# Kernel optimization log

Measured on AMD Instinct MI355X. Metric: run time of the kernel, lower is better.

Reference implementation:

```python
import jax, jax.numpy as jnp
import numpy as np

N, E, D = 20000, 640000, 128  # nodes, edges, hidden_nf
ED = 3  # edge_feat_nf (1 input col + distance col + geodesic col)
NORM_FACTOR = 100.0
NORM_CONST = 1.0
LN_EPS = 1e-5


def setup_inputs() -> dict:
    key = jax.random.key(0)
    ks = jax.random.split(key, 24)
    w = lambda k, s: (jax.random.normal(k, s, dtype=jnp.float32) * 0.1)
    inp = {
        "h": jax.random.normal(ks[0], (N, D), dtype=jnp.float32),
        "x": jax.random.normal(ks[1], (N, 3), dtype=jnp.float32),
        "edge_index": jax.random.randint(ks[2], (2, E), 0, N),
        "node_mask": jnp.ones((N, 1), jnp.float32),
        "edge_mask": jnp.ones((E, 1), jnp.float32),
        "edge_attr": jax.random.uniform(ks[3], (E, 1), dtype=jnp.float32),
        # GCLayer params
        "W_lin": w(ks[4], (D, D)), "b_lin": jnp.zeros((D,), jnp.float32),
        "We1": w(ks[5], (D + ED, D)), "be1": jnp.zeros((D,), jnp.float32),
        "We2": w(ks[6], (D, D)), "be2": jnp.zeros((D,), jnp.float32),
        "Wn1": w(ks[7], (D, D)), "bn1": jnp.zeros((D,), jnp.float32),
        "Wn2": w(ks[8], (D, D)), "bn2": jnp.zeros((D,), jnp.float32),
        "Wa1": w(ks[9], (2 * D + ED, D)), "ba1": jnp.zeros((D,), jnp.float32),
        "Wa2": w(ks[10], (D, 1)), "ba2": jnp.zeros((1,), jnp.float32),
        "ln_g": jnp.ones((D,), jnp.float32), "ln_b": jnp.zeros((D,), jnp.float32),
        # EquivariantUpdate coord_mlp params (last layer bias-free, gain 0.001)
        "Wc1": w(ks[11], (2 * D + ED, D)), "bc1": jnp.zeros((D,), jnp.float32),
        "Wc2": w(ks[12], (D, D)), "bc2": jnp.zeros((D,), jnp.float32),
        "Wc3": w(ks[13], (D, 1)) * 0.01,
    }
    return inp


def _forward(h, x, edge_index, node_mask, edge_mask, edge_attr,
             W_lin, b_lin, We1, be1, We2, be2, Wn1, bn1, Wn2, bn2,
             Wa1, ba1, Wa2, ba2, ln_g, ln_b, Wc1, bc1, Wc2, bc2, Wc3):
    silu = jax.nn.silu
    row, col = edge_index[0], edge_index[1]
    # coord2diff
    diff = x[row] - x[col]                                     # [E,3]
    radial = jnp.sum(diff * diff, axis=1, keepdims=True)
    dist = jnp.sqrt(radial + 1e-8)                             # [E,1]
    coord_diff = diff / (dist + NORM_CONST)
    e = jnp.concatenate([dist, edge_attr], axis=1)             # [E,2]
    # ---- GCLayer (Euclidean reduction of HGCLayer) ----
    hh = h @ W_lin + b_lin                                     # [N,D]
    hr, hc = hh[row], hh[col]
    geo = jnp.sqrt(jnp.sum((hr - hc) ** 2, axis=1, keepdims=True) + 1e-8)
    e3 = jnp.concatenate([e, geo], axis=1)                     # [E,3]
    att_in = jnp.concatenate([hr, hc, e3], axis=1)             # [E,2D+3]
    att = jax.nn.sigmoid(silu(att_in @ Wa1 + ba1) @ Wa2 + ba2) * edge_mask
    msg_in = jnp.concatenate([hc - hr, e3], axis=1)            # [E,D+3]
    msg = (silu(msg_in @ We1 + be1) @ We2 + be2) * att
    agg = jax.ops.segment_sum(msg, row, num_segments=hh.shape[0])  # [N,D]
    out = silu(agg @ Wn1 + bn1) @ Wn2 + bn2
    hh = hh + out
    mu = jnp.mean(hh, axis=-1, keepdims=True)
    var = jnp.mean((hh - mu) ** 2, axis=-1, keepdims=True)
    hh = (hh - mu) * jax.lax.rsqrt(var + LN_EPS) * ln_g + ln_b
    hh = silu(hh)
    # ---- EquivariantUpdate (tanh=False) ----
    cin = jnp.concatenate([hh[row], hh[col], e3], axis=1)      # [E,2D+3]
    m = silu(cin @ Wc1 + bc1)
    m = silu(m @ Wc2 + bc2)
    m = m @ Wc3                                                # [E,1]
    trans = coord_diff * m * edge_mask
    aggx = jax.ops.segment_sum(trans, row, num_segments=x.shape[0]) / NORM_FACTOR
    x_out = (x + aggx) * node_mask
    return hh, x_out


def reference(h, x, edge_index, node_mask, edge_mask, edge_attr,
              W_lin, b_lin, We1, be1, We2, be2, Wn1, bn1, Wn2, bn2,
              Wa1, ba1, Wa2, ba2, ln_g, ln_b, Wc1, bc1, Wc2, bc2, Wc3):
    return _forward(h, x, edge_index, node_mask, edge_mask, edge_attr,
                    W_lin, b_lin, We1, be1, We2, be2, Wn1, bn1, Wn2, bn2,
                    Wa1, ba1, Wa2, ba2, ln_g, ln_b, Wc1, bc1, Wc2, bc2, Wc3)
```

## Files before the change

kernel.cpp:

```cpp
#include <hip/hip_runtime.h>
#include <hip/hip_bf16.h>


#define D 128
#define RS 136

typedef unsigned short ushort;
typedef __attribute__((ext_vector_type(8))) short short8;
typedef __attribute__((ext_vector_type(4))) float f32x4;

__device__ __forceinline__ float rcpf(float x) { return __builtin_amdgcn_rcpf(x); }
__device__ __forceinline__ float siluf(float x) { return x * rcpf(1.0f + __expf(-x)); }
__device__ __forceinline__ float sigmf(float x) { return rcpf(1.0f + __expf(-x)); }
__device__ __forceinline__ ushort f2bs(float f) {
    __hip_bfloat16 b = __float2bfloat16(f);
    ushort u; __builtin_memcpy(&u, &b, 2); return u;
}
__device__ __forceinline__ unsigned pkbf(float lo, float hi) {
    __hip_bfloat162 h2 = __float22bfloat162_rn(make_float2(lo, hi));
    unsigned u; __builtin_memcpy(&u, &h2, 4); return u;
}
#define MFMA16(a, b, c) __builtin_amdgcn_mfma_f32_16x16x32_bf16((a), (b), (c), 0, 0, 0)

#define PWLIN 0
#define PWA1  5
#define PWE1  14
#define PWE2  19
#define PWN1  23
#define PWN2  28
#define PWC1  32
#define PWC2  41
#define NPACK 45

__global__ void k_zero(float* __restrict__ p, long n) {
    long i = (long)blockIdx.x * blockDim.x + threadIdx.x;
    long stride = (long)gridDim.x * blockDim.x;
    for (; i < n; i += stride) p[i] = 0.0f;
}

__global__ void k_hist(const int* __restrict__ eidx, int* __restrict__ cnt, int E) {
    int i = blockIdx.x * blockDim.x + threadIdx.x;
    const int stride = gridDim.x * blockDim.x;
    for (; i < E; i += stride) atomicAdd(&cnt[eidx[i]], 1);
}

__global__ __launch_bounds__(1024) void k_scan(const int* __restrict__ cnt,
                                               int* __restrict__ cur, int N) {
    __shared__ int part[1024];
    const int t = threadIdx.x;
    const int chunk = (N + 1023) / 1024;
    int s = 0;
    for (int k = 0; k < chunk; ++k) {
        const int i = t * chunk + k;
        if (i < N) s += cnt[i];
    }
    part[t] = s;
    __syncthreads();
    for (int d = 1; d < 1024; d <<= 1) {
        const int v = (t >= d) ? part[t - d] : 0;
        __syncthreads();
        part[t] += v;
        __syncthreads();
    }
    int base = (t == 0) ? 0 : part[t - 1];
    for (int k = 0; k < chunk; ++k) {
        const int i = t * chunk + k;
        if (i < N) { cur[i] = base; base += cnt[i]; }
    }
}

__global__ void k_scatter_build(
    const int* __restrict__ eidx, const float* __restrict__ x,
    const float* __restrict__ eattr, const float* __restrict__ emask,
    int* __restrict__ cur, float4* __restrict__ rec, int E) {
    int i = blockIdx.x * blockDim.x + threadIdx.x;
    const int stride = gridDim.x * blockDim.x;
    for (; i < E; i += stride) {
        const int r = eidx[i], c = eidx[E + i];
        const int p = atomicAdd(&cur[r], 1);
        const float dx = x[r * 3 + 0] - x[c * 3 + 0];
        const float dy = x[r * 3 + 1] - x[c * 3 + 1];
        const float dz = x[r * 3 + 2] - x[c * 3 + 2];
        const float dist = sqrtf(dx * dx + dy * dy + dz * dz + 1e-8f);
        const float inv = rcpf(dist + 1.0f);
        rec[2 * p + 0] = make_float4(__int_as_float(r), __int_as_float(c), dist, eattr[i]);
        rec[2 * p + 1] = make_float4(emask[i], dx * inv, dy * inv, dz * inv);
    }
}

__global__ __launch_bounds__(256) void k_packall(
    const float* __restrict__ W_lin, const float* __restrict__ b_lin,
    const float* __restrict__ Wa1, const float* __restrict__ ba1,
    const float* __restrict__ We1, const float* __restrict__ be1,
    const float* __restrict__ We2,
    const float* __restrict__ Wn1, const float* __restrict__ bn1,
    const float* __restrict__ Wn2,
    const float* __restrict__ Wc1, const float* __restrict__ bc1,
    const float* __restrict__ Wc2,
    ushort* __restrict__ pack) {
    const int b = blockIdx.x, t = threadIdx.x;
    const float* W = nullptr; const float* bias = nullptr;
    int kbase = 0, fold = 0, ext = 0, nW = 0;
    if (b < 5)       { W = W_lin; bias = b_lin; if (b == 4) { ext = 1; nW = 0; } else kbase = b * 32; }
    else if (b < 14) { int k = b - 5;  W = Wa1; bias = ba1; if (k == 8) { ext = 1; nW = 3; kbase = 256; } else { kbase = k * 32; fold = (k < 4); } }
    else if (b < 19) { int k = b - 14; W = We1; bias = be1; if (k == 4) { ext = 1; nW = 3; kbase = 128; } else kbase = k * 32; }
    else if (b < 23) { W = We2; kbase = (b - 19) * 32; }
    else if (b < 28) { int k = b - 23; W = Wn1; bias = bn1; if (k == 4) { ext = 1; nW = 0; } else kbase = k * 32; }
    else if (b < 32) { W = Wn2; kbase = (b - 28) * 32; }
    else if (b < 41) { int k = b - 32; W = Wc1; bias = bc1; if (k == 8) { ext = 1; nW = 3; kbase = 256; } else kbase = k * 32; }
    else             { W = Wc2; kbase = (b - 41) * 32; }
    ushort* dst = pack + (size_t)b * 4096;
#pragma unroll
    for (int i = 0; i < 16; ++i) {
        const int e = t + 256 * i;
        const int j = e & 7, lane = (e >> 3) & 63, nt = e >> 9;
        const int kl = (lane >> 4) * 8 + j;
        const int n = nt * 16 + (lane & 15);
        float v;
        if (!ext) {
            v = W[(kbase + kl) * D + n];
            if (fold) v += W[(kbase + kl + 128) * D + n];
        } else {
            v = (kl < nW) ? W[(kbase + kl) * D + n] : (kl == nW ? bias[n] : 0.0f);
        }
        dst[e] = f2bs(v);
    }
}

__global__ __launch_bounds__(256) void k_node_lin(
    const float* __restrict__ h, const ushort* __restrict__ pack,
    float* __restrict__ hh, ushort* __restrict__ hh1b, int N) {
    __shared__ ushort hs[64][RS];
    const int t = threadIdx.x, lane = t & 63, wave = t >> 6;
    const int quad = lane >> 4, l16 = lane & 15;
    const int mh = wave >> 1, nh = wave & 1;
    const int base = blockIdx.x * 64;

#pragma unroll
    for (int q = 0; q < 8; ++q) {
        const int f = t + 256 * q;
        const int row = f >> 5, c4 = (f & 31) << 2;
        const int node = base + row;
        float4 v = make_float4(0.f, 0.f, 0.f, 0.f);
        if (node < N) v = *(const float4*)(h + (size_t)node * D + c4);
        *(uint2*)&hs[row][c4] = make_uint2(pkbf(v.x, v.y), pkbf(v.z, v.w));
    }
    __syncthreads();

    short8 aext = (short8)0;
    if (quad == 0) aext[0] = (short)0x3F80;

    f32x4 acc[2][4] = {};
    const short8* pB = (const short8*)(pack + (size_t)PWLIN * 4096);
#pragma unroll
    for (int ks = 0; ks < 5; ++ks) {
        short8 bfr[4];
#pragma unroll
        for (int nt = 0; nt < 4; ++nt) bfr[nt] = pB[(ks * 8 + nh * 4 + nt) * 64 + lane];
#pragma unroll
        for (int mt = 0; mt < 2; ++mt) {
            const short8 a = (ks < 4) ? *(const short8*)&hs[mh * 32 + mt * 16 + l16][ks * 32 + quad * 8]
                                      : aext;
#pragma unroll
            for (int nt = 0; nt < 4; ++nt) acc[mt][nt] = MFMA16(a, bfr[nt], acc[mt][nt]);
        }
    }
#pragma unroll
    for (int mt = 0; mt < 2; ++mt)
#pragma unroll
        for (int reg = 0; reg < 4; ++reg) {
            const int g = base + mh * 32 + mt * 16 + quad * 4 + reg;
            if (g < N) {
#pragma unroll
                for (int nt = 0; nt < 4; ++nt) {
                    const int col = nh * 64 + nt * 16 + l16;
                    const float v = acc[mt][nt][reg];
                    hh[(size_t)g * D + col] = v;
                    hh1b[(size_t)g * D + col] = f2bs(v);
                }
            }
        }
}

__global__ __launch_bounds__(256) void k_edge1(
    const float4* __restrict__ rec,
    const ushort* __restrict__ hh1b, const ushort* __restrict__ pack,
    const float* __restrict__ Wa2f, const float* __restrict__ ba2f,
    const float* __restrict__ be2f,
    float* __restrict__ agg, float* __restrict__ geo_c, int E) {
    __shared__ ushort ab_s[2][32][RS];
    __shared__ float dist_s[32], attr_s[32], geo_s[32], att_s[32], em_s[32];
    __shared__ int node_s[32], col_s[32];
    __shared__ float attp_s[4][32];

    float (*msg_s)[130] = (float(*)[130])&ab_s[0][0][0];

    const int t = threadIdx.x, lane = t & 63, w = t >> 6;
    const int quad = lane >> 4, l16 = lane & 15;
    const int base = blockIdx.x * 32;

    if (t < 32) {
        const int i = base + t;
        int r = 0, c = 0; float dist = 0.f, at = 0.f, emv = 0.f;
        if (i < E) {
            const float4 ra = rec[2 * i + 0];
            const float4 rb = rec[2 * i + 1];
            r = __float_as_int(ra.x); c = __float_as_int(ra.y);
            dist = ra.z; at = ra.w; emv = rb.x;
        }
        node_s[t] = r; col_s[t] = c;
        dist_s[t] = dist; attr_s[t] = at; em_s[t] = emv;
    }
    float wa2[2], b3[2];
#pragma unroll
    for (int nt = 0; nt < 2; ++nt) {
        const int col = w * 32 + nt * 16 + l16;
        wa2[nt] = Wa2f[col]; b3[nt] = be2f[col];
    }
    __syncthreads();

    {
        const int g = t >> 4;
#pragma unroll
        for (int it = 0; it < 2; ++it) {
            const int e = g * 2 + it;
            const uint4 vr = *(const uint4*)(hh1b + (size_t)node_s[e] * D + l16 * 8);
            const uint4 vc = *(const uint4*)(hh1b + (size_t)col_s[e] * D + l16 * 8);
            *(uint4*)&ab_s[0][e][l16 * 8] = vr;
            const unsigned* pr = (const unsigned*)&vr;
            const unsigned* pc = (const unsigned*)&vc;
            float s = 0.f; unsigned dw[4];
#pragma unroll
            for (int q = 0; q < 4; ++q) {
                const float r0 = __uint_as_float(pr[q] << 16), r1 = __uint_as_float(pr[q] & 0xffff0000u);
                const float c0 = __uint_as_float(pc[q] << 16), c1 = __uint_as_float(pc[q] & 0xffff0000u);
                const float d0 = c0 - r0, d1 = c1 - r1;
                s += d0 * d0 + d1 * d1;
                dw[q] = pkbf(d0, d1);
            }
            *(uint4*)&ab_s[1][e][l16 * 8] = make_uint4(dw[0], dw[1], dw[2], dw[3]);
            s += __shfl_xor(s, 1); s += __shfl_xor(s, 2); s += __shfl_xor(s, 4); s += __shfl_xor(s, 8);
            if (l16 == 0) {
                const float gg = sqrtf(s + 1e-8f);
                geo_s[e] = gg;
                if (base + e < E) geo_c[base + e] = gg;
            }
        }
    }
    __syncthreads();

    short8 aext[2];
#pragma unroll
    for (int mt = 0; mt < 2; ++mt) {
        short8 v = (short8)0;
        if (quad == 0) {
            const int m = mt * 16 + l16;
            v[0] = (short)f2bs(dist_s[m]); v[1] = (short)f2bs(attr_s[m]);
            v[2] = (short)f2bs(geo_s[m]);  v[3] = (short)0x3F80;
        }
        aext[mt] = v;
    }

    f32x4 accA[2][2] = {}, accM[2][2] = {};
    {
        const short8* pA = (const short8*)(pack + (size_t)PWA1 * 4096);
        const short8* pM = (const short8*)(pack + (size_t)PWE1 * 4096);
#pragma unroll
        for (int ks = 0; ks < 9; ++ks) {
            const short8 bA0 = pA[(ks * 8 + w * 2 + 0) * 64 + lane];
            const short8 bA1 = pA[(ks * 8 + w * 2 + 1) * 64 + lane];
            short8 bM0 = (short8)0, bM1 = (short8)0;
            if (ks >= 4) {
                bM0 = pM[((ks - 4) * 8 + w * 2 + 0) * 64 + lane];
                bM1 = pM[((ks - 4) * 8 + w * 2 + 1) * 64 + lane];
            }
#pragma unroll
            for (int mt = 0; mt < 2; ++mt) {
                const short8 a = (ks < 4) ? *(const short8*)&ab_s[0][mt * 16 + l16][ks * 32 + quad * 8]
                               : (ks < 8) ? *(const short8*)&ab_s[1][mt * 16 + l16][(ks - 4) * 32 + quad * 8]
                                          : aext[mt];
                accA[mt][0] = MFMA16(a, bA0, accA[mt][0]);
                accA[mt][1] = MFMA16(a, bA1, accA[mt][1]);
                if (ks >= 4) {
                    accM[mt][0] = MFMA16(a, bM0, accM[mt][0]);
                    accM[mt][1] = MFMA16(a, bM1, accM[mt][1]);
                }
            }
        }
    }
#pragma unroll
    for (int mt = 0; mt < 2; ++mt)
#pragma unroll
        for (int reg = 0; reg < 4; ++reg) {
            float p = siluf(accA[mt][0][reg]) * wa2[0] + siluf(accA[mt][1][reg]) * wa2[1];
            p += __shfl_xor(p, 1); p += __shfl_xor(p, 2); p += __shfl_xor(p, 4); p += __shfl_xor(p, 8);
            if (l16 == 0) attp_s[w][mt * 16 + quad * 4 + reg] = p;
        }
    __syncthreads();

    if (t < 32)
        att_s[t] = sigmf(attp_s[0][t] + attp_s[1][t] + attp_s[2][t] + attp_s[3][t] + ba2f[0]) * em_s[t];
#pragma unroll
    for (int mt = 0; mt < 2; ++mt)
#pragma unroll
        for (int reg = 0; reg < 4; ++reg) {
            const int row = mt * 16 + quad * 4 + reg;
#pragma unroll
            for (int nt = 0; nt < 2; ++nt)
                ab_s[0][row][w * 32 + nt * 16 + l16] = f2bs(siluf(accM[mt][nt][reg]));
        }
    __syncthreads();

    f32x4 acc3[2][2] = {};
    {
        const short8* pB = (const short8*)(pack + (size_t)PWE2 * 4096);
#pragma unroll
        for (int ks = 0; ks < 4; ++ks) {
            const short8 b0 = pB[(ks * 8 + w * 2 + 0) * 64 + lane];
            const short8 b1 = pB[(ks * 8 + w * 2 + 1) * 64 + lane];
#pragma unroll
            for (int mt = 0; mt < 2; ++mt) {
                const short8 a = *(const short8*)&ab_s[0][mt * 16 + l16][ks * 32 + quad * 8];
                acc3[mt][0] = MFMA16(a, b0, acc3[mt][0]);
                acc3[mt][1] = MFMA16(a, b1, acc3[mt][1]);
            }
        }
    }
    __syncthreads();
#pragma unroll
    for (int mt = 0; mt < 2; ++mt)
#pragma unroll
        for (int reg = 0; reg < 4; ++reg) {
            const int row = mt * 16 + quad * 4 + reg;
            const float av = att_s[row];
#pragma unroll
            for (int nt = 0; nt < 2; ++nt)
                msg_s[row][w * 32 + nt * 16 + l16] = (acc3[mt][nt][reg] + b3[nt]) * av;
        }
    __syncthreads();

    {
        const int j = t & 127, h = t >> 7;
        float acc = 0.f;
        int rprev = node_s[h * 16];
#pragma unroll
        for (int k = 0; k < 16; ++k) {
            const int row = h * 16 + k;
            const int rn = node_s[row];
            if (rn != rprev) {
                atomicAdd(&agg[(size_t)rprev * D + j], acc);
                acc = 0.f; rprev = rn;
            }
            acc += msg_s[row][j];
        }
        atomicAdd(&agg[(size_t)rprev * D + j], acc);
    }
}

__global__ __launch_bounds__(256) void k_node2(
    const float* __restrict__ agg, float* hio,
    const ushort* __restrict__ pack,
    const float* __restrict__ bn2f,
    const float* __restrict__ ln_g, const float* __restrict__ ln_b,
    ushort* __restrict__ hh2b, int N) {
    __shared__ ushort ag_s[64][RS];
    __shared__ float redS[2][64], redQ[2][64];
    const int t = threadIdx.x, lane = t & 63, wave = t >> 6;
    const int quad = lane >> 4, l16 = lane & 15;
    const int mh = wave >> 1, nh = wave & 1;
    const int base = blockIdx.x * 64;

#pragma unroll
    for (int q = 0; q < 8; ++q) {
        const int f = t + 256 * q;
        const int row = f >> 5, c4 = (f & 31) << 2;
        const int node = base + row;
        float4 v = make_float4(0.f, 0.f, 0.f, 0.f);
        if (node < N) v = *(const float4*)(agg + (size_t)node * D + c4);
        *(uint2*)&ag_s[row][c4] = make_uint2(pkbf(v.x, v.y), pkbf(v.z, v.w));
    }
    float bn2[4], lg[4], lb[4];
#pragma unroll
    for (int nt = 0; nt < 4; ++nt) {
        const int col = nh * 64 + nt * 16 + l16;
        bn2[nt] = bn2f[col]; lg[nt] = ln_g[col]; lb[nt] = ln_b[col];
    }
    __syncthreads();

    short8 aext = (short8)0;
    if (quad == 0) aext[0] = (short)0x3F80;

    f32x4 acc[2][4] = {};
    {
        const short8* pB = (const short8*)(pack + (size_t)PWN1 * 4096);
#pragma unroll
        for (int ks = 0; ks < 5; ++ks) {
            short8 bfr[4];
#pragma unroll
            for (int nt = 0; nt < 4; ++nt) bfr[nt] = pB[(ks * 8 + nh * 4 + nt) * 64 + lane];
#pragma unroll
            for (int mt = 0; mt < 2; ++mt) {
                const short8 a = (ks < 4) ? *(const short8*)&ag_s[mh * 32 + mt * 16 + l16][ks * 32 + quad * 8]
                                          : aext;
#pragma unroll
                for (int nt = 0; nt < 4; ++nt) acc[mt][nt] = MFMA16(a, bfr[nt], acc[mt][nt]);
            }
        }
    }
    __syncthreads();
#pragma unroll
    for (int mt = 0; mt < 2; ++mt)
#pragma unroll
        for (int reg = 0; reg < 4; ++reg) {
            const int row = mh * 32 + mt * 16 + quad * 4 + reg;
#pragma unroll
            for (int nt = 0; nt < 4; ++nt)
                ag_s[row][nh * 64 + nt * 16 + l16] = f2bs(siluf(acc[mt][nt][reg]));
        }
    __syncthreads();

    {
        const short8* pB = (const short8*)(pack + (size_t)PWN2 * 4096);
#pragma unroll
        for (int mt = 0; mt < 2; ++mt)
#pragma unroll
            for (int nt = 0; nt < 4; ++nt) acc[mt][nt] = (f32x4)0.0f;
#pragma unroll
        for (int ks = 0; ks < 4; ++ks) {
            short8 bfr[4];
#pragma unroll
            for (int nt = 0; nt < 4; ++nt) bfr[nt] = pB[(ks * 8 + nh * 4 + nt) * 64 + lane];
#pragma unroll
            for (int mt = 0; mt < 2; ++mt) {
                const short8 a = *(const short8*)&ag_s[mh * 32 + mt * 16 + l16][ks * 32 + quad * 8];
#pragma unroll
                for (int nt = 0; nt < 4; ++nt) acc[mt][nt] = MFMA16(a, bfr[nt], acc[mt][nt]);
            }
        }
    }
#pragma unroll
    for (int mt = 0; mt < 2; ++mt)
#pragma unroll
        for (int reg = 0; reg < 4; ++reg) {
            const int row = mh * 32 + mt * 16 + quad * 4 + reg;
            const int g = base + row;
            float s = 0.f, qq = 0.f;
#pragma unroll
            for (int nt = 0; nt < 4; ++nt) {
                const int col = nh * 64 + nt * 16 + l16;
                float v = acc[mt][nt][reg] + bn2[nt];
                if (g < N) v += hio[(size_t)g * D + col];
                acc[mt][nt][reg] = v;
                s += v; qq += v * v;
            }
            s += __shfl_xor(s, 1); s += __shfl_xor(s, 2); s += __shfl_xor(s, 4); s += __shfl_xor(s, 8);
            qq += __shfl_xor(qq, 1); qq += __shfl_xor(qq, 2); qq += __shfl_xor(qq, 4); qq += __shfl_xor(qq, 8);
            if (l16 == 0) { redS[nh][row] = s; redQ[nh][row] = qq; }
        }
    __syncthreads();

#pragma unroll
    for (int mt = 0; mt < 2; ++mt)
#pragma unroll
        for (int reg = 0; reg < 4; ++reg) {
            const int row = mh * 32 + mt * 16 + quad * 4 + reg;
            const int g = base + row;
            const float mu = (redS[0][row] + redS[1][row]) * (1.0f / D);
            const float var = (redQ[0][row] + redQ[1][row]) * (1.0f / D) - mu * mu;
            const float rstd = rsqrtf(var + 1e-5f);
            if (g < N) {
#pragma unroll
                for (int nt = 0; nt < 4; ++nt) {
                    const int col = nh * 64 + nt * 16 + l16;
                    const float hn = (acc[mt][nt][reg] - mu) * rstd * lg[nt] + lb[nt];
                    const float o = siluf(hn);
                    hio[(size_t)g * D + col] = o;
                    hh2b[(size_t)g * D + col] = f2bs(o);
                }
            }
        }
}

__global__ __launch_bounds__(256) void k_edge2(
    const float4* __restrict__ rec, const float* __restrict__ geo_c,
    const ushort* __restrict__ hh2b, const ushort* __restrict__ pack,
    const float* __restrict__ bc2f, const float* __restrict__ Wc3f,
    float* __restrict__ aggx, int E) {
    __shared__ ushort ar_s[32][RS];
    __shared__ ushort ac_s[32][RS];
    __shared__ float dist_s[32], attr_s[32], geo_s[32], tr_s[32];
    __shared__ float cdx_s[32], cdy_s[32], cdz_s[32];
    __shared__ int node_s[32], col_s[32];
    __shared__ float mp_s[4][32];

    const int t = threadIdx.x, lane = t & 63, w = t >> 6;
    const int quad = lane >> 4, l16 = lane & 15;
    const int base = blockIdx.x * 32;

    if (t < 32) {
        const int i = base + t;
        int r = 0, c = 0;
        float dist = 1.f, geo = 0.f, at = 0.f, emv = 0.f, cdx = 0.f, cdy = 0.f, cdz = 0.f;
        if (i < E) {
            const float4 ra = rec[2 * i + 0];
            const float4 rb = rec[2 * i + 1];
            r = __float_as_int(ra.x); c = __float_as_int(ra.y);
            dist = ra.z; at = ra.w;
            emv = rb.x; cdx = rb.y; cdy = rb.z; cdz = rb.w;
            geo = geo_c[i];
        }
        node_s[t] = r; col_s[t] = c;
        dist_s[t] = dist; geo_s[t] = geo; attr_s[t] = at; tr_s[t] = emv;
        cdx_s[t] = cdx; cdy_s[t] = cdy; cdz_s[t] = cdz;
    }
    float bc2[2], wc3[2];
#pragma unroll
    for (int nt = 0; nt < 2; ++nt) {
        const int col = w * 32 + nt * 16 + l16;
        bc2[nt] = bc2f[col]; wc3[nt] = Wc3f[col];
    }
    __syncthreads();

    {
        const int g = t >> 4;
#pragma unroll
        for (int it = 0; it < 2; ++it) {
            const int e = g * 2 + it;
            *(uint4*)&ar_s[e][l16 * 8] = *(const uint4*)(hh2b + (size_t)node_s[e] * D + l16 * 8);
            *(uint4*)&ac_s[e][l16 * 8] = *(const uint4*)(hh2b + (size_t)col_s[e] * D + l16 * 8);
        }
    }
    __syncthreads();

    short8 aext[2];
#pragma unroll
    for (int mt = 0; mt < 2; ++mt) {
        short8 v = (short8)0;
        if (quad == 0) {
            const int m = mt * 16 + l16;
            v[0] = (short)f2bs(dist_s[m]); v[1] = (short)f2bs(attr_s[m]);
            v[2] = (short)f2bs(geo_s[m]);  v[3] = (short)0x3F80;
        }
        aext[mt] = v;
    }

    {
        f32x4 acc[2][2] = {};
        const short8* pB = (const short8*)(pack + (size_t)PWC1 * 4096);
#pragma unroll
        for (int ks = 0; ks < 9; ++ks) {
            const short8 b0 = pB[(ks * 8 + w * 2 + 0) * 64 + lane];
            const short8 b1 = pB[(ks * 8 + w * 2 + 1) * 64 + lane];
#pragma unroll
            for (int mt = 0; mt < 2; ++mt) {
                const short8 a = (ks < 4) ? *(const short8*)&ar_s[mt * 16 + l16][ks * 32 + quad * 8]
                               : (ks < 8) ? *(const short8*)&ac_s[mt * 16 + l16][(ks - 4) * 32 + quad * 8]
                                          : aext[mt];
                acc[mt][0] = MFMA16(a, b0, acc[mt][0]);
                acc[mt][1] = MFMA16(a, b1, acc[mt][1]);
            }
        }
        __syncthreads();
#pragma unroll
        for (int mt = 0; mt < 2; ++mt)
#pragma unroll
            for (int reg = 0; reg < 4; ++reg) {
                const int row = mt * 16 + quad * 4 + reg;
#pragma unroll
                for (int nt = 0; nt < 2; ++nt)
                    ar_s[row][w * 32 + nt * 16 + l16] = f2bs(siluf(acc[mt][nt][reg]));
            }
    }
    __syncthreads();

    {
        f32x4 acc[2][2] = {};
        const short8* pB = (const short8*)(pack + (size_t)PWC2 * 4096);
#pragma unroll
        for (int ks = 0; ks < 4; ++ks) {
            const short8 b0 = pB[(ks * 8 + w * 2 + 0) * 64 + lane];
            const short8 b1 = pB[(ks * 8 + w * 2 + 1) * 64 + lane];
#pragma unroll
            for (int mt = 0; mt < 2; ++mt) {
                const short8 a = *(const short8*)&ar_s[mt * 16 + l16][ks * 32 + quad * 8];
                acc[mt][0] = MFMA16(a, b0, acc[mt][0]);
                acc[mt][1] = MFMA16(a, b1, acc[mt][1]);
            }
        }
#pragma unroll
        for (int mt = 0; mt < 2; ++mt)
#pragma unroll
            for (int reg = 0; reg < 4; ++reg) {
                float p = siluf(acc[mt][0][reg] + bc2[0]) * wc3[0]
                        + siluf(acc[mt][1][reg] + bc2[1]) * wc3[1];
                p += __shfl_xor(p, 1); p += __shfl_xor(p, 2); p += __shfl_xor(p, 4); p += __shfl_xor(p, 8);
                if (l16 == 0) mp_s[w][mt * 16 + quad * 4 + reg] = p;
            }
    }
    __syncthreads();

    if (t < 32) {
        const float m = mp_s[0][t] + mp_s[1][t] + mp_s[2][t] + mp_s[3][t];
        tr_s[t] = m * tr_s[t];
        if (base + t >= E) tr_s[t] = 0.f;
    }
    __syncthreads();

    if (t < 3) {
        const float* cds = (t == 0) ? cdx_s : (t == 1) ? cdy_s : cdz_s;
        float acc = 0.f;
        int rprev = node_s[0];
#pragma unroll
        for (int k = 0; k < 32; ++k) {
            const int rn = node_s[k];
            if (rn != rprev) {
                atomicAdd(&aggx[rprev * 4 + t], acc);
                acc = 0.f; rprev = rn;
            }
            acc += cds[k] * tr_s[k];
        }
        atomicAdd(&aggx[rprev * 4 + t], acc);
    }
}

__global__ void k_coord(const float* __restrict__ x, const float* __restrict__ nmask,
                        const float* __restrict__ aggx, float* __restrict__ out_x, int N) {
    const int idx = blockIdx.x * blockDim.x + threadIdx.x;
    if (idx >= N * 3) return;
    const int i = idx / 3, d = idx - i * 3;
    out_x[idx] = (x[idx] + aggx[i * 4 + d] * (1.0f / 100.0f)) * nmask[i];
}

extern "C" void kernel_launch(void* const* d_in, const int* in_sizes, int n_in,
                              void* d_out, int out_size, void* d_ws, size_t ws_size,
                              hipStream_t stream) {
    const float* h     = (const float*)d_in[0];
    const float* x     = (const float*)d_in[1];
    const int*   eidx  = (const int*)d_in[2];
    const float* nmask = (const float*)d_in[3];
    const float* emask = (const float*)d_in[4];
    const float* eattr = (const float*)d_in[5];
    const float* W_lin = (const float*)d_in[6];
    const float* b_lin = (const float*)d_in[7];
    const float* We1   = (const float*)d_in[8];
    const float* be1   = (const float*)d_in[9];
    const float* We2   = (const float*)d_in[10];
    const float* be2   = (const float*)d_in[11];
    const float* Wn1   = (const float*)d_in[12];
    const float* bn1   = (const float*)d_in[13];
    const float* Wn2   = (const float*)d_in[14];
    const float* bn2   = (const float*)d_in[15];
    const float* Wa1   = (const float*)d_in[16];
    const float* ba1   = (const float*)d_in[17];
    const float* Wa2   = (const float*)d_in[18];
    const float* ba2   = (const float*)d_in[19];
    const float* ln_g  = (const float*)d_in[20];
    const float* ln_b  = (const float*)d_in[21];
    const float* Wc1   = (const float*)d_in[22];
    const float* bc1   = (const float*)d_in[23];
    const float* Wc2   = (const float*)d_in[24];
    const float* bc2   = (const float*)d_in[25];
    const float* Wc3   = (const float*)d_in[26];

    const int N = in_sizes[0] / D;
    const int E = in_sizes[2] / 2;

    char* wp = (char*)d_ws;
    auto take = [&](size_t bytes) -> void* {
        void* p = wp; wp += (bytes + 255) & ~(size_t)255; return p;
    };
    float*  agg   = (float*)take((size_t)N * D * 4);
    float*  aggx  = (float*)take((size_t)N * 4 * 4);
    int*    cnt   = (int*)take((size_t)N * 4);
    int*    cur   = (int*)take((size_t)N * 4);
    float4* rec   = (float4*)take((size_t)E * 32);
    float*  geo_c = (float*)take((size_t)E * 4);
    ushort* hh1b  = (ushort*)take((size_t)N * D * 2);
    ushort* hh2b  = (ushort*)take((size_t)N * D * 2);
    ushort* pack  = (ushort*)take((size_t)NPACK * 4096 * 2);

    float* out_h = (float*)d_out;
    float* out_x = out_h + (size_t)N * D;

    const int EB = (E + 31) / 32;
    const int NB = (N + 63) / 64;
    const long zn = ((char*)(cnt + N) - (char*)agg) / 4;

    k_zero<<<2048, 256, 0, stream>>>(agg, zn);
    k_packall<<<NPACK, 256, 0, stream>>>(W_lin, b_lin, Wa1, ba1, We1, be1, We2,
                                         Wn1, bn1, Wn2, Wc1, bc1, Wc2, pack);
    k_hist<<<1024, 256, 0, stream>>>(eidx, cnt, E);
    k_scan<<<1, 1024, 0, stream>>>(cnt, cur, N);
    k_scatter_build<<<1024, 256, 0, stream>>>(eidx, x, eattr, emask, cur, rec, E);
    k_node_lin<<<NB, 256, 0, stream>>>(h, pack, out_h, hh1b, N);
    k_edge1<<<EB, 256, 0, stream>>>(rec, hh1b, pack, Wa2, ba2, be2, agg, geo_c, E);
    k_node2<<<NB, 256, 0, stream>>>(agg, out_h, pack, bn2, ln_g, ln_b, hh2b, N);
    k_edge2<<<EB, 256, 0, stream>>>(rec, geo_c, hh2b, pack, bc2, Wc3, aggx, E);
    k_coord<<<(N * 3 + 255) / 256, 256, 0, stream>>>(x, nmask, aggx, out_x, N);
}
```

Measured before the change: 546.3 us.

## Double edge tile to 64 per block in both edge kernels

Both edge kernels now process 64 edges per block instead of 32, so each weight fragment loaded from global memory feeds twice as many MFMA tiles. The edge1 segmented scatter-add gets a fast path that does one atomic per column when all 32 rows of a half-tile share a source node, and edge2 splits its coordinate reduction across two thread groups. Launch bounds request 4 blocks per CU, and f2bs is rewritten through the packed bf16 conversion. The cost is more shared memory and accumulator registers per block, which may limit occupancy, and half as many blocks in the grid.

```diff
diff --git a/kernel.cpp b/kernel.cpp
--- a/kernel.cpp
+++ b/kernel.cpp
@@ -12,13 +12,12 @@
 __device__ __forceinline__ float rcpf(float x) { return __builtin_amdgcn_rcpf(x); }
 __device__ __forceinline__ float siluf(float x) { return x * rcpf(1.0f + __expf(-x)); }
 __device__ __forceinline__ float sigmf(float x) { return rcpf(1.0f + __expf(-x)); }
-__device__ __forceinline__ ushort f2bs(float f) {
-    __hip_bfloat16 b = __float2bfloat16(f);
-    ushort u; __builtin_memcpy(&u, &b, 2); return u;
-}
 __device__ __forceinline__ unsigned pkbf(float lo, float hi) {
     __hip_bfloat162 h2 = __float22bfloat162_rn(make_float2(lo, hi));
     unsigned u; __builtin_memcpy(&u, &h2, 4); return u;
+}
+__device__ __forceinline__ ushort f2bs(float f) {
+    return (ushort)pkbf(f, f);
 }
 #define MFMA16(a, b, c) __builtin_amdgcn_mfma_f32_16x16x32_bf16((a), (b), (c), 0, 0, 0)
 
@@ -182,24 +181,24 @@
         }
 }
 
-__global__ __launch_bounds__(256) void k_edge1(
+__global__ __launch_bounds__(256, 4) void k_edge1(
     const float4* __restrict__ rec,
     const ushort* __restrict__ hh1b, const ushort* __restrict__ pack,
     const float* __restrict__ Wa2f, const float* __restrict__ ba2f,
     const float* __restrict__ be2f,
     float* __restrict__ agg, float* __restrict__ geo_c, int E) {
-    __shared__ ushort ab_s[2][32][RS];
-    __shared__ float dist_s[32], attr_s[32], geo_s[32], att_s[32], em_s[32];
-    __shared__ int node_s[32], col_s[32];
-    __shared__ float attp_s[4][32];
+    __shared__ ushort ab_s[2][64][RS];
+    __shared__ float dist_s[64], attr_s[64], geo_s[64], att_s[64], em_s[64];
+    __shared__ int node_s[64], col_s[64];
+    __shared__ float attp_s[4][64];
 
     float (*msg_s)[130] = (float(*)[130])&ab_s[0][0][0];
 
     const int t = threadIdx.x, lane = t & 63, w = t >> 6;
     const int quad = lane >> 4, l16 = lane & 15;
-    const int base = blockIdx.x * 32;
-
-    if (t < 32) {
+    const int base = blockIdx.x * 64;
+
+    if (t < 64) {
         const int i = base + t;
         int r = 0, c = 0; float dist = 0.f, at = 0.f, emv = 0.f;
         if (i < E) {
@@ -222,8 +221,8 @@
     {
         const int g = t >> 4;
 #pragma unroll
-        for (int it = 0; it < 2; ++it) {
-            const int e = g * 2 + it;
+        for (int it = 0; it < 4; ++it) {
+            const int e = g * 4 + it;
             const uint4 vr = *(const uint4*)(hh1b + (size_t)node_s[e] * D + l16 * 8);
             const uint4 vc = *(const uint4*)(hh1b + (size_t)col_s[e] * D + l16 * 8);
             *(uint4*)&ab_s[0][e][l16 * 8] = vr;
@@ -249,9 +248,9 @@
     }
     __syncthreads();
 
-    short8 aext[2];
-#pragma unroll
-    for (int mt = 0; mt < 2; ++mt) {
+    short8 aext[4];
+#pragma unroll
+    for (int mt = 0; mt < 4; ++mt) {
         short8 v = (short8)0;
         if (quad == 0) {
             const int m = mt * 16 + l16;
@@ -261,7 +260,7 @@
         aext[mt] = v;
     }
 
-    f32x4 accA[2][2] = {}, accM[2][2] = {};
+    f32x4 accA[4][2] = {}, accM[4][2] = {};
     {
         const short8* pA = (const short8*)(pack + (size_t)PWA1 * 4096);
         const short8* pM = (const short8*)(pack + (size_t)PWE1 * 4096);
@@ -275,7 +274,7 @@
                 bM1 = pM[((ks - 4) * 8 + w * 2 + 1) * 64 + lane];
             }
 #pragma unroll
-            for (int mt = 0; mt < 2; ++mt) {
+            for (int mt = 0; mt < 4; ++mt) {
                 const short8 a = (ks < 4) ? *(const short8*)&ab_s[0][mt * 16 + l16][ks * 32 + quad * 8]
                                : (ks < 8) ? *(const short8*)&ab_s[1][mt * 16 + l16][(ks - 4) * 32 + quad * 8]
                                           : aext[mt];
@@ -289,7 +288,7 @@
         }
     }
 #pragma unroll
-    for (int mt = 0; mt < 2; ++mt)
+    for (int mt = 0; mt < 4; ++mt)
 #pragma unroll
         for (int reg = 0; reg < 4; ++reg) {
             float p = siluf(accA[mt][0][reg]) * wa2[0] + siluf(accA[mt][1][reg]) * wa2[1];
@@ -298,10 +297,10 @@
         }
     __syncthreads();
 
-    if (t < 32)
+    if (t < 64)
         att_s[t] = sigmf(attp_s[0][t] + attp_s[1][t] + attp_s[2][t] + attp_s[3][t] + ba2f[0]) * em_s[t];
 #pragma unroll
-    for (int mt = 0; mt < 2; ++mt)
+    for (int mt = 0; mt < 4; ++mt)
 #pragma unroll
         for (int reg = 0; reg < 4; ++reg) {
             const int row = mt * 16 + quad * 4 + reg;
@@ -311,7 +310,7 @@
         }
     __syncthreads();
 
-    f32x4 acc3[2][2] = {};
+    f32x4 acc3[4][2] = {};
     {
         const short8* pB = (const short8*)(pack + (size_t)PWE2 * 4096);
 #pragma unroll
@@ -319,7 +318,7 @@
             const short8 b0 = pB[(ks * 8 + w * 2 + 0) * 64 + lane];
             const short8 b1 = pB[(ks * 8 + w * 2 + 1) * 64 + lane];
 #pragma unroll
-            for (int mt = 0; mt < 2; ++mt) {
+            for (int mt = 0; mt < 4; ++mt) {
                 const short8 a = *(const short8*)&ab_s[0][mt * 16 + l16][ks * 32 + quad * 8];
                 acc3[mt][0] = MFMA16(a, b0, acc3[mt][0]);
                 acc3[mt][1] = MFMA16(a, b1, acc3[mt][1]);
@@ -328,7 +327,7 @@
     }
     __syncthreads();
 #pragma unroll
-    for (int mt = 0; mt < 2; ++mt)
+    for (int mt = 0; mt < 4; ++mt)
 #pragma unroll
         for (int reg = 0; reg < 4; ++reg) {
             const int row = mt * 16 + quad * 4 + reg;
@@ -341,19 +340,27 @@
 
     {
         const int j = t & 127, h = t >> 7;
-        float acc = 0.f;
-        int rprev = node_s[h * 16];
-#pragma unroll
-        for (int k = 0; k < 16; ++k) {
-            const int row = h * 16 + k;
-            const int rn = node_s[row];
-            if (rn != rprev) {
-                atomicAdd(&agg[(size_t)rprev * D + j], acc);
-                acc = 0.f; rprev = rn;
-            }
-            acc += msg_s[row][j];
-        }
-        atomicAdd(&agg[(size_t)rprev * D + j], acc);
+        const int r0 = node_s[h * 32];
+        if (r0 == node_s[h * 32 + 31]) {
+            float acc = 0.f;
+#pragma unroll
+            for (int k = 0; k < 32; ++k) acc += msg_s[h * 32 + k][j];
+            atomicAdd(&agg[(size_t)r0 * D + j], acc);
+        } else {
+            float acc = 0.f;
+            int rprev = r0;
+#pragma unroll
+            for (int k = 0; k < 32; ++k) {
+                const int row = h * 32 + k;
+                const int rn = node_s[row];
+                if (rn != rprev) {
+                    atomicAdd(&agg[(size_t)rprev * D + j], acc);
+                    acc = 0.f; rprev = rn;
+                }
+                acc += msg_s[row][j];
+            }
+            atomicAdd(&agg[(size_t)rprev * D + j], acc);
+        }
     }
 }
 
@@ -481,23 +488,23 @@
         }
 }
 
-__global__ __launch_bounds__(256) void k_edge2(
+__global__ __launch_bounds__(256, 4) void k_edge2(
     const float4* __restrict__ rec, const float* __restrict__ geo_c,
     const ushort* __restrict__ hh2b, const ushort* __restrict__ pack,
     const float* __restrict__ bc2f, const float* __restrict__ Wc3f,
     float* __restrict__ aggx, int E) {
-    __shared__ ushort ar_s[32][RS];
-    __shared__ ushort ac_s[32][RS];
-    __shared__ float dist_s[32], attr_s[32], geo_s[32], tr_s[32];
-    __shared__ float cdx_s[32], cdy_s[32], cdz_s[32];
-    __shared__ int node_s[32], col_s[32];
-    __shared__ float mp_s[4][32];
+    __shared__ ushort ar_s[64][RS];
+    __shared__ ushort ac_s[64][RS];
+    __shared__ float dist_s[64], attr_s[64], geo_s[64], tr_s[64];
+    __shared__ float cdx_s[64], cdy_s[64], cdz_s[64];
+    __shared__ int node_s[64], col_s[64];
+    __shared__ float mp_s[4][64];
 
     const int t = threadIdx.x, lane = t & 63, w = t >> 6;
     const int quad = lane >> 4, l16 = lane & 15;
-    const int base = blockIdx.x * 32;
-
-    if (t < 32) {
+    const int base = blockIdx.x * 64;
+
+    if (t < 64) {
         const int i = base + t;
         int r = 0, c = 0;
         float dist = 1.f, geo = 0.f, at = 0.f, emv = 0.f, cdx = 0.f, cdy = 0.f, cdz = 0.f;
@@ -524,17 +531,17 @@
     {
         const int g = t >> 4;
 #pragma unroll
-        for (int it = 0; it < 2; ++it) {
-            const int e = g * 2 + it;
+        for (int it = 0; it < 4; ++it) {
+            const int e = g * 4 + it;
             *(uint4*)&ar_s[e][l16 * 8] = *(const uint4*)(hh2b + (size_t)node_s[e] * D + l16 * 8);
             *(uint4*)&ac_s[e][l16 * 8] = *(const uint4*)(hh2b + (size_t)col_s[e] * D + l16 * 8);
         }
     }
     __syncthreads();
 
-    short8 aext[2];
-#pragma unroll
-    for (int mt = 0; mt < 2; ++mt) {
+    short8 aext[4];
+#pragma unroll
+    for (int mt = 0; mt < 4; ++mt) {
         short8 v = (short8)0;
         if (quad == 0) {
             const int m = mt * 16 + l16;
@@ -545,14 +552,14 @@
     }
 
     {
-        f32x4 acc[2][2] = {};
+        f32x4 acc[4][2] = {};
         const short8* pB = (const short8*)(pack + (size_t)PWC1 * 4096);
 #pragma unroll
         for (int ks = 0; ks < 9; ++ks) {
             const short8 b0 = pB[(ks * 8 + w * 2 + 0) * 64 + lane];
             const short8 b1 = pB[(ks * 8 + w * 2 + 1) * 64 + lane];
 #pragma unroll
-            for (int mt = 0; mt < 2; ++mt) {
+            for (int mt = 0; mt < 4; ++mt) {
                 const short8 a = (ks < 4) ? *(const short8*)&ar_s[mt * 16 + l16][ks * 32 + quad * 8]
                                : (ks < 8) ? *(const short8*)&ac_s[mt * 16 + l16][(ks - 4) * 32 + quad * 8]
                                           : aext[mt];
@@ -562,7 +569,7 @@
         }
         __syncthreads();
 #pragma unroll
-        for (int mt = 0; mt < 2; ++mt)
+        for (int mt = 0; mt < 4; ++mt)
 #pragma unroll
             for (int reg = 0; reg < 4; ++reg) {
                 const int row = mt * 16 + quad * 4 + reg;
@@ -574,21 +581,21 @@
     __syncthreads();
 
     {
-        f32x4 acc[2][2] = {};
+        f32x4 acc[4][2] = {};
         const short8* pB = (const short8*)(pack + (size_t)PWC2 * 4096);
 #pragma unroll
         for (int ks = 0; ks < 4; ++ks) {
             const short8 b0 = pB[(ks * 8 + w * 2 + 0) * 64 + lane];
             const short8 b1 = pB[(ks * 8 + w * 2 + 1) * 64 + lane];
 #pragma unroll
-            for (int mt = 0; mt < 2; ++mt) {
+            for (int mt = 0; mt < 4; ++mt) {
                 const short8 a = *(const short8*)&ar_s[mt * 16 + l16][ks * 32 + quad * 8];
                 acc[mt][0] = MFMA16(a, b0, acc[mt][0]);
                 acc[mt][1] = MFMA16(a, b1, acc[mt][1]);
             }
         }
 #pragma unroll
-        for (int mt = 0; mt < 2; ++mt)
+        for (int mt = 0; mt < 4; ++mt)
 #pragma unroll
             for (int reg = 0; reg < 4; ++reg) {
                 float p = siluf(acc[mt][0][reg] + bc2[0]) * wc3[0]
@@ -599,27 +606,31 @@
     }
     __syncthreads();
 
-    if (t < 32) {
+    if (t < 64) {
         const float m = mp_s[0][t] + mp_s[1][t] + mp_s[2][t] + mp_s[3][t];
         tr_s[t] = m * tr_s[t];
         if (base + t >= E) tr_s[t] = 0.f;
     }
     __syncthreads();
 
-    if (t < 3) {
-        const float* cds = (t == 0) ? cdx_s : (t == 1) ? cdy_s : cdz_s;
-        float acc = 0.f;
-        int rprev = node_s[0];
-#pragma unroll
-        for (int k = 0; k < 32; ++k) {
-            const int rn = node_s[k];
-            if (rn != rprev) {
-                atomicAdd(&aggx[rprev * 4 + t], acc);
-                acc = 0.f; rprev = rn;
-            }
-            acc += cds[k] * tr_s[k];
-        }
-        atomicAdd(&aggx[rprev * 4 + t], acc);
+    {
+        const int h = t >> 7, tt = t & 127;
+        if (tt < 3) {
+            const float* cds = (tt == 0) ? cdx_s : (tt == 1) ? cdy_s : cdz_s;
+            float acc = 0.f;
+            int rprev = node_s[h * 32];
+#pragma unroll
+            for (int k = 0; k < 32; ++k) {
+                const int row = h * 32 + k;
+                const int rn = node_s[row];
+                if (rn != rprev) {
+                    atomicAdd(&aggx[rprev * 4 + tt], acc);
+                    acc = 0.f; rprev = rn;
+                }
+                acc += cds[row] * tr_s[row];
+            }
+            atomicAdd(&aggx[rprev * 4 + tt], acc);
+        }
     }
 }
 
@@ -682,7 +693,7 @@
     float* out_h = (float*)d_out;
     float* out_x = out_h + (size_t)N * D;
 
-    const int EB = (E + 31) / 32;
+    const int EB = (E + 63) / 64;
     const int NB = (N + 63) / 64;
     const long zn = ((char*)(cnt + N) - (char*)agg) / 4;
 
```

Measured after the change: 549.2 us. Within noise of the previous version (+0.5%).
